# Kernel tuning notes

Measured on AMD Instinct MI355X. Metric: run time of the kernel, lower is better.

Reference implementation:

```python
import jax, jax.numpy as jnp
import numpy as np

N_NODES = 50000
N_EDGES = 1600000
NEG_SLOPE = 0.2


def _gat_layer(x, src, dst, W, a_src, a_dst, b, n_nodes):
    # PyG GATConv (heads=1, concat=True): h = xW; e_ij = LeakyReLU(a_src.h_j + a_dst.h_i)
    # alpha = softmax over incoming edges of each target i; out_i = sum_j alpha_ij h_j + b
    h = x @ W                                   # [N, out]
    alpha_src = h @ a_src                        # [N]
    alpha_dst = h @ a_dst                        # [N]
    e = alpha_src[src] + alpha_dst[dst]          # [E]
    e = jnp.where(e > 0, e, NEG_SLOPE * e)       # leaky_relu(0.2)
    m = jax.ops.segment_max(e, dst, num_segments=n_nodes)   # per-target max
    ex = jnp.exp(e - m[dst])
    denom = jax.ops.segment_sum(ex, dst, num_segments=n_nodes)
    alpha = ex / (denom[dst] + 1e-16)            # [E]
    out = jax.ops.segment_sum(alpha[:, None] * h[src], dst, num_segments=n_nodes)
    return out + b


def setup_inputs() -> dict:
    key = jax.random.key(0)
    ks = jax.random.split(key, 16)
    hid, out_dim, in_dim = 128, 5, 13
    x = jax.random.normal(ks[0], (N_NODES, in_dim), dtype=jnp.float32)
    edge_index = jax.random.randint(ks[1], (2, N_EDGES), 0, N_NODES, dtype=jnp.int64)
    s = 0.1
    return {
        "x": x,
        "edge_index": edge_index,
        "W1": jax.random.normal(ks[2], (in_dim, hid), dtype=jnp.float32) * s,
        "a_src1": jax.random.normal(ks[3], (hid,), dtype=jnp.float32) * s,
        "a_dst1": jax.random.normal(ks[4], (hid,), dtype=jnp.float32) * s,
        "b1": jnp.zeros((hid,), dtype=jnp.float32),
        "W2": jax.random.normal(ks[5], (hid, hid), dtype=jnp.float32) * s,
        "a_src2": jax.random.normal(ks[6], (hid,), dtype=jnp.float32) * s,
        "a_dst2": jax.random.normal(ks[7], (hid,), dtype=jnp.float32) * s,
        "b2": jnp.zeros((hid,), dtype=jnp.float32),
        "W3": jax.random.normal(ks[8], (hid, out_dim), dtype=jnp.float32) * s,
        "a_src3": jax.random.normal(ks[9], (out_dim,), dtype=jnp.float32) * s,
        "a_dst3": jax.random.normal(ks[10], (out_dim,), dtype=jnp.float32) * s,
        "b3": jnp.zeros((out_dim,), dtype=jnp.float32),
    }


def reference(x, edge_index, W1, a_src1, a_dst1, b1, W2, a_src2, a_dst2, b2,
              W3, a_src3, a_dst3, b3):
    n = x.shape[0]
    # GATConv add_self_loops=True: append (i, i) edges
    loops = jnp.arange(n, dtype=edge_index.dtype)
    src = jnp.concatenate([edge_index[0], loops])
    dst = jnp.concatenate([edge_index[1], loops])
    h = _gat_layer(x, src, dst, W1, a_src1, a_dst1, b1, n)
    h = jax.nn.relu(h)  # dropout identity in eval mode
    h = _gat_layer(h, src, dst, W2, a_src2, a_dst2, b2, n)
    h = jax.nn.relu(h)
    h = _gat_layer(h, src, dst, W3, a_src3, a_dst3, b3, n)
    return jax.nn.log_softmax(h, axis=1)
```

## Files before the change

### kernel.cpp

```cpp
#include <hip/hip_runtime.h>
#include <hip/hip_bf16.h>


#define LEAKY(e) ((e) > 0.f ? (e) : 0.2f * (e))
#define CAPB 6144
__device__ inline float clamp30(float e) { return fminf(fmaxf(e, -30.f), 30.f); }
__device__ inline float expc(float e) { return __expf(clamp30(LEAKY(e))); }

__device__ inline float ldany(const void* p, int bf, int i) {
    return bf ? __bfloat162float(((const __hip_bfloat16*)p)[i])
              : ((const float*)p)[i];
}
__device__ inline int ldidx(const void* p, int i64, long long i) {
    return i64 ? (int)(((const unsigned int*)p)[2 * i])
               : ((const int*)p)[i];
}

__device__ inline float bflo(unsigned int w) { return __uint_as_float(w << 16); }
__device__ inline float bfhi(unsigned int w) { return __uint_as_float(w & 0xffff0000u); }
__device__ inline unsigned short bfbits(float a) {
    __hip_bfloat16 x = __float2bfloat16(a);
    unsigned short u; __builtin_memcpy(&u, &x, 2); return u;
}
__device__ inline unsigned int packbf(float a, float b) {
    return (unsigned int)bfbits(a) | ((unsigned int)bfbits(b) << 16);
}

typedef __attribute__((ext_vector_type(8))) short short8;
typedef __attribute__((ext_vector_type(4))) float f32x4;

__global__ void detect_kernel(const void* W1, const void* ei, int* flags) {
    if (threadIdx.x == 0 && blockIdx.x == 0) {
        const unsigned int* w = (const unsigned int*)W1;
        int c = 0;
        for (int i = 0; i < 64; i++) {
            unsigned int e = (w[i] >> 7) & 0xFFu;
            if (e >= 0x70u && e <= 0x7Fu) c++;
        }
        flags[0] = (c >= 32) ? 1 : 0;
        const unsigned int* q = (const unsigned int*)ei;
        int z = 0;
        for (int i = 0; i < 64; i++)
            if (q[2 * i + 1] == 0u) z++;
        flags[1] = (z >= 32) ? 1 : 0;
    }
}


__global__ __launch_bounds__(256) void zero_ints(int* p, int n) {
    int i = blockIdx.x * 256 + threadIdx.x;
    if (i < n) p[i] = 0;
}

__global__ __launch_bounds__(256) void scatter1(
    const void* __restrict__ ei, const int* __restrict__ flags,
    int* __restrict__ gcur, unsigned int* __restrict__ pairbuf, int E, int NBUK)
{
    __shared__ unsigned int ebuf[6400];
    __shared__ int hist[512];
    __shared__ int wbase[512];
    const int i64 = flags[1];
    const int tid = threadIdx.x, blk = blockIdx.x;
    const int chunk = (E + 255) / 256;
    const int e0 = blk * chunk, e1 = min(e0 + chunk, E);
    for (int sub = e0; sub < e1; sub += 6400) {
        const int cnt = min(6400, e1 - sub);
        for (int i = tid; i < NBUK; i += 256) hist[i] = 0;
        __syncthreads();
        for (int i = tid; i < cnt; i += 256) {
            int s = ldidx(ei, i64, sub + i);
            int d = ldidx(ei, i64, (long long)E + sub + i);
            ebuf[i] = ((unsigned int)d << 16) | (unsigned int)s;
            atomicAdd(&hist[d >> 7], 1);
        }
        __syncthreads();
        for (int b = tid; b < NBUK; b += 256) {
            int h = hist[b];
            wbase[b] = (h > 0) ? (b * CAPB + atomicAdd(&gcur[b], h)) : 0;
            hist[b] = 0;
        }
        __syncthreads();
        for (int i = tid; i < cnt; i += 256) {
            unsigned int w = ebuf[i];
            int b = (int)(w >> 23);
            int p = atomicAdd(&hist[b], 1);
            pairbuf[wbase[b] + p] = w;
        }
        __syncthreads();
    }
}

__global__ __launch_bounds__(512) void sortB2_scan(
    const int* __restrict__ gcur, int* __restrict__ bucketBase, int NBUK)
{
    __shared__ int wt[8];
    __shared__ int wbase[8];
    __shared__ int total_s;
    const int tid = threadIdx.x, lane = tid & 63, wid = tid >> 6;
    int v = (tid < NBUK) ? gcur[tid] : 0;
    int x = v;
#pragma unroll
    for (int o = 1; o < 64; o <<= 1) {
        int y = __shfl_up(x, o);
        if (lane >= o) x += y;
    }
    if (lane == 63) wt[wid] = x;
    __syncthreads();
    if (tid == 0) {
        int s = 0;
#pragma unroll
        for (int i = 0; i < 8; i++) { wbase[i] = s; s += wt[i]; }
        total_s = s;
    }
    __syncthreads();
    if (tid < NBUK) bucketBase[tid] = x - v + wbase[wid];
    if (tid == 0) bucketBase[NBUK] = total_s;
}

__global__ __launch_bounds__(256) void sortD_bin(
    const unsigned int* __restrict__ pairbuf, const int* __restrict__ bucketBase,
    int* __restrict__ rowptr, unsigned short* __restrict__ ssrc,
    int N, int NBUK)
{
    __shared__ int cnt[128];
    __shared__ int cur2[128];
    __shared__ int wt1;
    const int b = blockIdx.x;
    const int tid = threadIdx.x, lane = tid & 63;
    const int e0 = bucketBase[b], e1 = bucketBase[b + 1];
    const int nloc = e1 - e0;
    const unsigned int* pb = pairbuf + (size_t)b * CAPB;
    if (tid < 128) cnt[tid] = 0;
    __syncthreads();
    for (int i = tid; i < nloc; i += 256)
        atomicAdd(&cnt[(pb[i] >> 16) & 127], 1);
    __syncthreads();
    if (tid < 128) {
        int v = cnt[tid];
        int x = v;
#pragma unroll
        for (int o = 1; o < 64; o <<= 1) {
            int y = __shfl_up(x, o);
            if (lane >= o) x += y;
        }
        if (tid == 63) wt1 = x;
        __syncthreads();
        if (tid >= 64) x += wt1;
        int pfx = x - v;
        cur2[tid] = pfx;
        int node = b * 128 + tid;
        if (node < N) rowptr[node] = e0 + pfx;
    } else {
        __syncthreads();
    }
    if (b == NBUK - 1 && tid == 0) rowptr[N] = e1;
    __syncthreads();
    for (int i = tid; i < nloc; i += 256) {
        unsigned int w = pb[i];
        int p = atomicAdd(&cur2[(w >> 16) & 127], 1);
        ssrc[e0 + p] = (unsigned short)(w & 0xFFFFu);
    }
}


__global__ __launch_bounds__(256) void node_prep13(
    const void* __restrict__ xin, const void* __restrict__ Wg,
    const void* __restrict__ asg, const void* __restrict__ adg,
    const int* __restrict__ flags,
    unsigned int* __restrict__ h2, float* __restrict__ asrc,
    float* __restrict__ adst, int N)
{
    const int bf = flags[0];
    __shared__ float Wlds[13 * 128];
    for (int i = threadIdx.x; i < 13 * 128; i += 256)
        Wlds[i] = ldany(Wg, bf, i);
    __syncthreads();
    const int lane = threadIdx.x & 63;
    int wave = (blockIdx.x * 256 + threadIdx.x) >> 6;
    int nw = (gridDim.x * 256) >> 6;
    float a0 = ldany(asg, bf, 2 * lane), a1 = ldany(asg, bf, 2 * lane + 1);
    float d0 = ldany(adg, bf, 2 * lane), d1 = ldany(adg, bf, 2 * lane + 1);
    for (int n = wave; n < N; n += nw) {
        float x0 = (lane < 13) ? ldany(xin, bf, n * 13 + lane) : 0.f;
        float s0 = 0.f, s1 = 0.f;
#pragma unroll
        for (int k = 0; k < 13; k++) {
            float xv = __shfl(x0, k);
            s0 += xv * Wlds[k * 128 + 2 * lane];
            s1 += xv * Wlds[k * 128 + 2 * lane + 1];
        }
        float pa = s0 * a0 + s1 * a1;
        float pd = s0 * d0 + s1 * d1;
#pragma unroll
        for (int o = 32; o > 0; o >>= 1) {
            pa += __shfl_xor(pa, o);
            pd += __shfl_xor(pd, o);
        }
        if (lane == 0) { asrc[n] = pa; adst[n] = pd; }
        h2[(size_t)n * 64 + lane] = packbf(s0, s1);
    }
}

__global__ __launch_bounds__(256) void gemm_mfma(
    const float* __restrict__ X, const void* __restrict__ Wg,
    const void* __restrict__ asg, const void* __restrict__ adg,
    const int* __restrict__ flags, unsigned int* __restrict__ h2,
    float* __restrict__ asrc, float* __restrict__ adst, int N)
{
    const int bf = flags[0];
    __shared__ unsigned short A_s[64 * 136];
    __shared__ unsigned short B_s[128 * 136];
    const int tid = threadIdx.x;
    const int nb0 = blockIdx.x * 64;

#pragma unroll
    for (int it = 0; it < 16; it++) {
        int f = it * 256 + tid;
        int k = f >> 5, ng = (f & 31) * 4;
        if (!bf) {
            float4 v = *(const float4*)((const float*)Wg + k * 128 + ng);
            B_s[(ng + 0) * 136 + k] = bfbits(v.x);
            B_s[(ng + 1) * 136 + k] = bfbits(v.y);
            B_s[(ng + 2) * 136 + k] = bfbits(v.z);
            B_s[(ng + 3) * 136 + k] = bfbits(v.w);
        } else {
            const unsigned short* W16 = (const unsigned short*)Wg;
            B_s[(ng + 0) * 136 + k] = W16[k * 128 + ng + 0];
            B_s[(ng + 1) * 136 + k] = W16[k * 128 + ng + 1];
            B_s[(ng + 2) * 136 + k] = W16[k * 128 + ng + 2];
            B_s[(ng + 3) * 136 + k] = W16[k * 128 + ng + 3];
        }
    }
#pragma unroll
    for (int it = 0; it < 8; it++) {
        int f = it * 256 + tid;
        int n = f >> 5, g = f & 31;
        int node = min(nb0 + n, N - 1);
        float4 v = *(const float4*)&X[(size_t)node * 128 + g * 4];
        unsigned int* dst = (unsigned int*)&A_s[n * 136 + g * 4];
        dst[0] = packbf(v.x, v.y);
        dst[1] = packbf(v.z, v.w);
    }
    __syncthreads();

    const int wv = tid >> 6;
    const int lane = tid & 63;
    const int m = lane & 15, quad = lane >> 4;

    f32x4 acc[8];
#pragma unroll
    for (int c = 0; c < 8; c++) acc[c] = (f32x4){0.f, 0.f, 0.f, 0.f};

#pragma unroll
    for (int q = 0; q < 4; q++) {
        short8 a = *(const short8*)&A_s[(wv * 16 + m) * 136 + q * 32 + quad * 8];
#pragma unroll
        for (int c = 0; c < 8; c++) {
            short8 b = *(const short8*)&B_s[(c * 16 + m) * 136 + q * 32 + quad * 8];
            acc[c] = __builtin_amdgcn_mfma_f32_16x16x32_bf16(a, b, acc[c], 0, 0, 0);
        }
    }

    float asv[8], adv[8];
#pragma unroll
    for (int c = 0; c < 8; c++) {
        asv[c] = ldany(asg, bf, c * 16 + m);
        adv[c] = ldany(adg, bf, c * 16 + m);
    }
    unsigned short* h2u = (unsigned short*)h2;
#pragma unroll
    for (int reg = 0; reg < 4; reg++) {
        int node = nb0 + wv * 16 + quad * 4 + reg;
        float pa = 0.f, pd = 0.f;
#pragma unroll
        for (int c = 0; c < 8; c++) {
            float v = acc[c][reg];
            pa += v * asv[c];
            pd += v * adv[c];
            if (node < N) h2u[(size_t)node * 128 + c * 16 + m] = bfbits(v);
        }
#pragma unroll
        for (int o = 1; o < 16; o <<= 1) {
            pa += __shfl_xor(pa, o);
            pd += __shfl_xor(pd, o);
        }
        if (node < N && m == 0) { asrc[node] = pa; adst[node] = pd; }
    }
}

__global__ __launch_bounds__(256) void proj7(
    const float* __restrict__ X, const void* __restrict__ W3,
    const void* __restrict__ as3, const void* __restrict__ ad3,
    const int* __restrict__ flags, float* __restrict__ h3p,
    float* __restrict__ asrc, float* __restrict__ adst, int N)
{
    const int bf = flags[0];
    __shared__ float Wp[128 * 8];
    __shared__ float xs[256 * 33];
    const int tid = threadIdx.x;
    for (int i = tid; i < 128 * 8; i += 256) {
        int k = i >> 3, j = i & 7;
        float v = 0.f;
        if (j < 5) v = ldany(W3, bf, k * 5 + j);
        else if (j == 5) v = ldany(as3, bf, k);
        else if (j == 6) v = ldany(ad3, bf, k);
        Wp[i] = v;
    }
    const int nb0 = blockIdx.x * 256;
    float acc[7] = {0.f, 0.f, 0.f, 0.f, 0.f, 0.f, 0.f};
    for (int kc = 0; kc < 128; kc += 32) {
        __syncthreads();
#pragma unroll
        for (int it = 0; it < 32; it++) {
            int f = it * 256 + tid;
            int row = f >> 5, k = f & 31;
            int node = nb0 + row;
            xs[row * 33 + k] = (node < N) ? X[(size_t)node * 128 + kc + k] : 0.f;
        }
        __syncthreads();
#pragma unroll
        for (int k = 0; k < 32; k++) {
            float xv = xs[tid * 33 + k];
            float4 w0 = *(float4*)&Wp[(kc + k) * 8];
            float4 w1 = *(float4*)&Wp[(kc + k) * 8 + 4];
            acc[0] += xv * w0.x; acc[1] += xv * w0.y; acc[2] += xv * w0.z;
            acc[3] += xv * w0.w; acc[4] += xv * w1.x; acc[5] += xv * w1.y;
            acc[6] += xv * w1.z;
        }
    }
    int node = nb0 + tid;
    if (node < N) {
        float4 o0 = {acc[0], acc[1], acc[2], acc[3]};
        float4 o1 = {acc[4], 0.f, 0.f, 0.f};
        *(float4*)&h3p[(size_t)node * 8] = o0;
        *(float4*)&h3p[(size_t)node * 8 + 4] = o1;
        asrc[node] = acc[5];
        adst[node] = acc[6];
    }
}


__device__ inline int rdl(int v, int j) { return __builtin_amdgcn_readlane(v, j); }
__device__ inline float rdlf(float v, int j) {
    return __uint_as_float((unsigned int)__builtin_amdgcn_readlane((int)__float_as_uint(v), j));
}

__global__ __launch_bounds__(256) void agg_fused128(
    const int* __restrict__ rowptr, const unsigned short* __restrict__ ssrc,
    const unsigned int* __restrict__ h2, const float* __restrict__ asrc,
    const float* __restrict__ adst, const void* __restrict__ bias,
    const int* __restrict__ flags, float* __restrict__ feat, int N)
{
    const int bf = flags[0];
    const int lane = threadIdx.x & 63;
    int wave = (blockIdx.x * 256 + threadIdx.x) >> 6;
    int nw = (gridDim.x * 256) >> 6;
    const float bx = ldany(bias, bf, 2 * lane);
    const float by = ldany(bias, bf, 2 * lane + 1);
    const unsigned ul = (unsigned)lane;

    for (int n = wave; n < N; n += nw) {
        float ad = adst[n];
        float wself = expc(asrc[n] + ad);
        unsigned int hw = h2[((unsigned)n << 6) | ul];
        float accx = wself * bflo(hw), accy = wself * bfhi(hw);
        float wpart = (lane == 0) ? wself : 0.f;
        const int start = rowptr[n], end = rowptr[n + 1];
        for (int base = start; base < end; base += 64) {
            int sl = 0;
            float wl = 0.f;
            if (base + lane < end) {
                sl = (int)ssrc[base + lane];
                wl = expc(asrc[sl] + ad);
            }
            wpart += wl;
            const int cnt = min(64, end - base);
            int j = 0;
            for (; j + 16 <= cnt; j += 16) {
                unsigned int u[16];
                float w[16];
#pragma unroll
                for (int t = 0; t < 16; t++) {
                    unsigned s = (unsigned)rdl(sl, j + t);
                    u[t] = h2[(s << 6) | ul];
                }
#pragma unroll
                for (int t = 0; t < 16; t++) w[t] = rdlf(wl, j + t);
#pragma unroll
                for (int t = 0; t < 16; t++) {
                    accx += w[t] * bflo(u[t]);
                    accy += w[t] * bfhi(u[t]);
                }
            }
            for (; j + 8 <= cnt; j += 8) {
                unsigned int u[8];
                float w[8];
#pragma unroll
                for (int t = 0; t < 8; t++) {
                    unsigned s = (unsigned)rdl(sl, j + t);
                    u[t] = h2[(s << 6) | ul];
                }
#pragma unroll
                for (int t = 0; t < 8; t++) w[t] = rdlf(wl, j + t);
#pragma unroll
                for (int t = 0; t < 8; t++) {
                    accx += w[t] * bflo(u[t]);
                    accy += w[t] * bfhi(u[t]);
                }
            }
            for (; j < cnt; j++) {
                unsigned s = (unsigned)rdl(sl, j);
                float w = rdlf(wl, j);
                unsigned int ww = h2[(s << 6) | ul];
                accx += w * bflo(ww);
                accy += w * bfhi(ww);
            }
        }
        float wsum = wpart;
#pragma unroll
        for (int o = 32; o > 0; o >>= 1) wsum += __shfl_xor(wsum, o);
        float inv = 1.f / (wsum + 1e-16f);
        float2 ov = {fmaxf(accx * inv + bx, 0.f), fmaxf(accy * inv + by, 0.f)};
        *(float2*)&feat[(size_t)n * 128 + 2 * lane] = ov;
    }
}

__global__ __launch_bounds__(256) void agg_fused5(
    const int* __restrict__ rowptr, const unsigned short* __restrict__ ssrc,
    const float* __restrict__ h3p, const float* __restrict__ asrc,
    const float* __restrict__ adst, const void* __restrict__ b3,
    const int* __restrict__ flags, float* __restrict__ out, int N)
{
    const int bf = flags[0];
    const int lane = threadIdx.x & 63;
    int wave = (blockIdx.x * 256 + threadIdx.x) >> 6;
    int nw = (gridDim.x * 256) >> 6;

    for (int n = wave; n < N; n += nw) {
        float ad = adst[n];
        float a0 = 0.f, a1 = 0.f, a2 = 0.f, a3 = 0.f, a4 = 0.f, wsum = 0.f;
        if (lane == 0) {
            float w = expc(asrc[n] + ad);
            wsum = w;
            float4 v = *(const float4*)&h3p[(unsigned)n * 8u];
            float v4 = h3p[(unsigned)n * 8u + 4u];
            a0 = w * v.x; a1 = w * v.y; a2 = w * v.z; a3 = w * v.w; a4 = w * v4;
        }
        const int start = rowptr[n], end = rowptr[n + 1];
        for (int i = start + lane; i < end; i += 64) {
            unsigned s = (unsigned)ssrc[i];
            float w = expc(asrc[s] + ad);
            float4 v = *(const float4*)&h3p[s * 8u];
            float v4 = h3p[s * 8u + 4u];
            wsum += w;
            a0 += w * v.x; a1 += w * v.y; a2 += w * v.z; a3 += w * v.w; a4 += w * v4;
        }
#pragma unroll
        for (int o = 32; o > 0; o >>= 1) {
            a0 += __shfl_xor(a0, o); a1 += __shfl_xor(a1, o); a2 += __shfl_xor(a2, o);
            a3 += __shfl_xor(a3, o); a4 += __shfl_xor(a4, o); wsum += __shfl_xor(wsum, o);
        }
        if (lane == 0) {
            float inv = 1.f / (wsum + 1e-16f);
            float v0 = a0 * inv + ldany(b3, bf, 0);
            float v1 = a1 * inv + ldany(b3, bf, 1);
            float v2 = a2 * inv + ldany(b3, bf, 2);
            float v3 = a3 * inv + ldany(b3, bf, 3);
            float v4 = a4 * inv + ldany(b3, bf, 4);
            float m = fmaxf(fmaxf(fmaxf(v0, v1), fmaxf(v2, v3)), v4);
            float s = __expf(v0 - m) + __expf(v1 - m) + __expf(v2 - m)
                    + __expf(v3 - m) + __expf(v4 - m);
            float lse = m + __logf(s);
            out[n * 5 + 0] = v0 - lse; out[n * 5 + 1] = v1 - lse;
            out[n * 5 + 2] = v2 - lse; out[n * 5 + 3] = v3 - lse;
            out[n * 5 + 4] = v4 - lse;
        }
    }
}

extern "C" void kernel_launch(void* const* d_in, const int* in_sizes, int n_in,
                              void* d_out, int out_size, void* d_ws, size_t ws_size,
                              hipStream_t stream)
{
    const void* x  = d_in[0];
    const void* ei = d_in[1];
    const void* W1 = d_in[2];
    const void* as1= d_in[3];
    const void* ad1= d_in[4];
    const void* b1 = d_in[5];
    const void* W2 = d_in[6];
    const void* as2= d_in[7];
    const void* ad2= d_in[8];
    const void* b2 = d_in[9];
    const void* W3 = d_in[10];
    const void* as3= d_in[11];
    const void* ad3= d_in[12];
    const void* b3 = d_in[13];

    const int N = in_sizes[0] / 13;
    const int E = in_sizes[1] / 2;
    const int NBUK = (N + 127) / 128;

    float* ws    = (float*)d_ws;
    float* feat  = ws;
    unsigned int* h2 = (unsigned int*)(feat + (size_t)N * 128);
    float* asrc  = (float*)(h2 + (size_t)N * 64);
    float* adst  = asrc + N;
    float* h3p   = adst + N;
    int*   rowptr= (int*)(h3p + (size_t)N * 8);
    int*   bucketBase = rowptr + N + 1;
    int*   gcur  = bucketBase + NBUK + 1;
    unsigned int* pairbuf = (unsigned int*)(gcur + NBUK);
    unsigned short* ssrc16 = (unsigned short*)(pairbuf + (size_t)NBUK * CAPB);
    int*   flags = (int*)(ssrc16 + E);

    const int wb = (N + 3) / 4;
    const int gb = (N + 63) / 64;
    const int pb = (N + 255) / 256;

    detect_kernel<<<1, 64, 0, stream>>>(W1, ei, flags);

    zero_ints<<<(NBUK + 255) / 256, 256, 0, stream>>>(gcur, NBUK);
    scatter1<<<256, 256, 0, stream>>>(ei, flags, gcur, pairbuf, E, NBUK);
    sortB2_scan<<<1, 512, 0, stream>>>(gcur, bucketBase, NBUK);
    sortD_bin<<<NBUK, 256, 0, stream>>>(pairbuf, bucketBase, rowptr, ssrc16, N, NBUK);

    node_prep13<<<1024, 256, 0, stream>>>(x, W1, as1, ad1, flags, h2, asrc, adst, N);
    agg_fused128<<<wb, 256, 0, stream>>>(rowptr, ssrc16, h2, asrc, adst, b1, flags, feat, N);

    gemm_mfma<<<gb, 256, 0, stream>>>(feat, W2, as2, ad2, flags, h2, asrc, adst, N);
    agg_fused128<<<wb, 256, 0, stream>>>(rowptr, ssrc16, h2, asrc, adst, b2, flags, feat, N);

    proj7<<<pb, 256, 0, stream>>>(feat, W3, as3, ad3, flags, h3p, asrc, adst, N);
    agg_fused5<<<wb, 256, 0, stream>>>(rowptr, ssrc16, h3p, asrc, adst, b3, flags,
                                       (float*)d_out, N);
}
```

Measured before the change: 340.3 us.

## Replace capped bucket scatter with hist-prefix-scatter sort, pack bf16 weight with src index

The edge bucketing changes from a fixed-capacity per-bucket buffer filled through global atomics to a three-pass counting sort: per-block histograms, a per-bucket prefix over blocks, then a scatter into exact offsets. This removes the CAPB overflow risk and the padded pairbuf, at the cost of reading the edge list twice and launching extra kernels. In the aggregation kernel, the attention weight is rounded to bf16 and packed with the 16-bit source index into one register, so each neighbour needs a single readlane instead of two. This lowers weight precision, and the middle unroll step drops from 8 to 4.

```diff
diff --git a/kernel.cpp b/kernel.cpp
--- a/kernel.cpp
+++ b/kernel.cpp
@@ -3,7 +3,6 @@
 
 
 #define LEAKY(e) ((e) > 0.f ? (e) : 0.2f * (e))
-#define CAPB 6144
 __device__ inline float clamp30(float e) { return fminf(fmaxf(e, -30.f), 30.f); }
 __device__ inline float expc(float e) { return __expf(clamp30(LEAKY(e))); }
 
@@ -47,57 +46,60 @@
 }
 
 
-__global__ __launch_bounds__(256) void zero_ints(int* p, int n) {
-    int i = blockIdx.x * 256 + threadIdx.x;
-    if (i < n) p[i] = 0;
-}
-
-__global__ __launch_bounds__(256) void scatter1(
+__global__ __launch_bounds__(256) void sortA_hist(
     const void* __restrict__ ei, const int* __restrict__ flags,
-    int* __restrict__ gcur, unsigned int* __restrict__ pairbuf, int E, int NBUK)
-{
-    __shared__ unsigned int ebuf[6400];
+    int* __restrict__ blockHist, int E, int NBUK)
+{
     __shared__ int hist[512];
-    __shared__ int wbase[512];
     const int i64 = flags[1];
     const int tid = threadIdx.x, blk = blockIdx.x;
+    for (int i = tid; i < NBUK; i += 256) hist[i] = 0;
+    __syncthreads();
     const int chunk = (E + 255) / 256;
     const int e0 = blk * chunk, e1 = min(e0 + chunk, E);
-    for (int sub = e0; sub < e1; sub += 6400) {
-        const int cnt = min(6400, e1 - sub);
-        for (int i = tid; i < NBUK; i += 256) hist[i] = 0;
-        __syncthreads();
-        for (int i = tid; i < cnt; i += 256) {
-            int s = ldidx(ei, i64, sub + i);
-            int d = ldidx(ei, i64, (long long)E + sub + i);
-            ebuf[i] = ((unsigned int)d << 16) | (unsigned int)s;
-            atomicAdd(&hist[d >> 7], 1);
-        }
-        __syncthreads();
-        for (int b = tid; b < NBUK; b += 256) {
-            int h = hist[b];
-            wbase[b] = (h > 0) ? (b * CAPB + atomicAdd(&gcur[b], h)) : 0;
-            hist[b] = 0;
-        }
-        __syncthreads();
-        for (int i = tid; i < cnt; i += 256) {
-            unsigned int w = ebuf[i];
-            int b = (int)(w >> 23);
-            int p = atomicAdd(&hist[b], 1);
-            pairbuf[wbase[b] + p] = w;
-        }
-        __syncthreads();
-    }
+    for (int t = e0 + tid; t < e1; t += 256) {
+        int d = ldidx(ei, i64, (long long)E + t);
+        atomicAdd(&hist[d >> 7], 1);
+    }
+    __syncthreads();
+    for (int i = tid; i < NBUK; i += 256)
+        blockHist[blk * NBUK + i] = hist[i];
+}
+
+__global__ __launch_bounds__(256) void sortB_prefix(
+    int* __restrict__ blockHist, int* __restrict__ bucketBase, int NBUK)
+{
+    __shared__ int wt[4];
+    __shared__ int wbase[4];
+    const int b = blockIdx.x;
+    const int tid = threadIdx.x, lane = tid & 63, wid = tid >> 6;
+    int v = blockHist[tid * NBUK + b];
+    int x = v;
+#pragma unroll
+    for (int o = 1; o < 64; o <<= 1) {
+        int y = __shfl_up(x, o);
+        if (lane >= o) x += y;
+    }
+    if (lane == 63) wt[wid] = x;
+    __syncthreads();
+    if (tid == 0) {
+        int s = 0;
+#pragma unroll
+        for (int i = 0; i < 4; i++) { wbase[i] = s; s += wt[i]; }
+        bucketBase[b] = s;
+    }
+    __syncthreads();
+    blockHist[tid * NBUK + b] = x - v + wbase[wid];
 }
 
 __global__ __launch_bounds__(512) void sortB2_scan(
-    const int* __restrict__ gcur, int* __restrict__ bucketBase, int NBUK)
+    int* __restrict__ bucketBase, int NBUK)
 {
     __shared__ int wt[8];
     __shared__ int wbase[8];
     __shared__ int total_s;
     const int tid = threadIdx.x, lane = tid & 63, wid = tid >> 6;
-    int v = (tid < NBUK) ? gcur[tid] : 0;
+    int v = (tid < NBUK) ? bucketBase[tid] : 0;
     int x = v;
 #pragma unroll
     for (int o = 1; o < 64; o <<= 1) {
@@ -117,10 +119,30 @@
     if (tid == 0) bucketBase[NBUK] = total_s;
 }
 
+__global__ __launch_bounds__(256) void sortC_scatter(
+    const void* __restrict__ ei, const int* __restrict__ flags,
+    const int* __restrict__ blockHist, const int* __restrict__ bucketBase,
+    unsigned int* __restrict__ pairbuf, int E, int NBUK)
+{
+    __shared__ int cur[512];
+    const int i64 = flags[1];
+    const int tid = threadIdx.x, blk = blockIdx.x;
+    for (int i = tid; i < NBUK; i += 256)
+        cur[i] = blockHist[blk * NBUK + i] + bucketBase[i];
+    __syncthreads();
+    const int chunk = (E + 255) / 256;
+    const int e0 = blk * chunk, e1 = min(e0 + chunk, E);
+    for (int t = e0 + tid; t < e1; t += 256) {
+        int s = ldidx(ei, i64, t);
+        int d = ldidx(ei, i64, (long long)E + t);
+        int pos = atomicAdd(&cur[d >> 7], 1);
+        pairbuf[pos] = ((unsigned int)(d & 127) << 16) | (unsigned int)s;
+    }
+}
+
 __global__ __launch_bounds__(256) void sortD_bin(
     const unsigned int* __restrict__ pairbuf, const int* __restrict__ bucketBase,
-    int* __restrict__ rowptr, unsigned short* __restrict__ ssrc,
-    int N, int NBUK)
+    int* __restrict__ rowptr, unsigned short* __restrict__ ssrc, int N, int NBUK)
 {
     __shared__ int cnt[128];
     __shared__ int cur2[128];
@@ -128,12 +150,10 @@
     const int b = blockIdx.x;
     const int tid = threadIdx.x, lane = tid & 63;
     const int e0 = bucketBase[b], e1 = bucketBase[b + 1];
-    const int nloc = e1 - e0;
-    const unsigned int* pb = pairbuf + (size_t)b * CAPB;
     if (tid < 128) cnt[tid] = 0;
     __syncthreads();
-    for (int i = tid; i < nloc; i += 256)
-        atomicAdd(&cnt[(pb[i] >> 16) & 127], 1);
+    for (int i = e0 + tid; i < e1; i += 256)
+        atomicAdd(&cnt[pairbuf[i] >> 16], 1);
     __syncthreads();
     if (tid < 128) {
         int v = cnt[tid];
@@ -155,9 +175,9 @@
     }
     if (b == NBUK - 1 && tid == 0) rowptr[N] = e1;
     __syncthreads();
-    for (int i = tid; i < nloc; i += 256) {
-        unsigned int w = pb[i];
-        int p = atomicAdd(&cur2[(w >> 16) & 127], 1);
+    for (int i = e0 + tid; i < e1; i += 256) {
+        unsigned int w = pairbuf[i];
+        int p = atomicAdd(&cur2[w >> 16], 1);
         ssrc[e0 + p] = (unsigned short)(w & 0xFFFFu);
     }
 }
@@ -340,9 +360,8 @@
 }
 
 
-__device__ inline int rdl(int v, int j) { return __builtin_amdgcn_readlane(v, j); }
-__device__ inline float rdlf(float v, int j) {
-    return __uint_as_float((unsigned int)__builtin_amdgcn_readlane((int)__float_as_uint(v), j));
+__device__ inline unsigned rdlu(unsigned v, int j) {
+    return (unsigned)__builtin_amdgcn_readlane((int)v, j);
 }
 
 __global__ __launch_bounds__(256) void agg_fused128(
@@ -367,51 +386,55 @@
         float wpart = (lane == 0) ? wself : 0.f;
         const int start = rowptr[n], end = rowptr[n + 1];
         for (int base = start; base < end; base += 64) {
-            int sl = 0;
-            float wl = 0.f;
+            unsigned pkl = 0;
             if (base + lane < end) {
-                sl = (int)ssrc[base + lane];
-                wl = expc(asrc[sl] + ad);
+                unsigned s = (unsigned)ssrc[base + lane];
+                float wl = expc(asrc[s] + ad);
+                unsigned wb = ((unsigned)bfbits(wl)) << 16;
+                wpart += __uint_as_float(wb);
+                pkl = wb | s;
             }
-            wpart += wl;
             const int cnt = min(64, end - base);
             int j = 0;
             for (; j + 16 <= cnt; j += 16) {
-                unsigned int u[16];
-                float w[16];
+                unsigned pk[16];
+                unsigned u[16];
+#pragma unroll
+                for (int t = 0; t < 16; t++) pk[t] = rdlu(pkl, j + t);
 #pragma unroll
                 for (int t = 0; t < 16; t++) {
-                    unsigned s = (unsigned)rdl(sl, j + t);
-                    u[t] = h2[(s << 6) | ul];
+                    const unsigned int* row = h2 + ((pk[t] & 0xFFFFu) << 6);
+                    u[t] = row[ul];
                 }
 #pragma unroll
-                for (int t = 0; t < 16; t++) w[t] = rdlf(wl, j + t);
-#pragma unroll
                 for (int t = 0; t < 16; t++) {
-                    accx += w[t] * bflo(u[t]);
-                    accy += w[t] * bfhi(u[t]);
+                    float w = __uint_as_float(pk[t] & 0xFFFF0000u);
+                    accx += w * bflo(u[t]);
+                    accy += w * bfhi(u[t]);
                 }
             }
-            for (; j + 8 <= cnt; j += 8) {
-                unsigned int u[8];
-                float w[8];
-#pragma unroll
-                for (int t = 0; t < 8; t++) {
-                    unsigned s = (unsigned)rdl(sl, j + t);
-                    u[t] = h2[(s << 6) | ul];
+            for (; j + 4 <= cnt; j += 4) {
+                unsigned pk[4];
+                unsigned u[4];
+#pragma unroll
+                for (int t = 0; t < 4; t++) pk[t] = rdlu(pkl, j + t);
+#pragma unroll
+                for (int t = 0; t < 4; t++) {
+                    const unsigned int* row = h2 + ((pk[t] & 0xFFFFu) << 6);
+                    u[t] = row[ul];
                 }
 #pragma unroll
-                for (int t = 0; t < 8; t++) w[t] = rdlf(wl, j + t);
-#pragma unroll
-                for (int t = 0; t < 8; t++) {
-                    accx += w[t] * bflo(u[t]);
-                    accy += w[t] * bfhi(u[t]);
+                for (int t = 0; t < 4; t++) {
+                    float w = __uint_as_float(pk[t] & 0xFFFF0000u);
+                    accx += w * bflo(u[t]);
+                    accy += w * bfhi(u[t]);
                 }
             }
             for (; j < cnt; j++) {
-                unsigned s = (unsigned)rdl(sl, j);
-                float w = rdlf(wl, j);
-                unsigned int ww = h2[(s << 6) | ul];
+                unsigned pk = rdlu(pkl, j);
+                const unsigned int* row = h2 + ((pk & 0xFFFFu) << 6);
+                unsigned ww = row[ul];
+                float w = __uint_as_float(pk & 0xFFFF0000u);
                 accx += w * bflo(ww);
                 accy += w * bfhi(ww);
             }
@@ -509,9 +532,9 @@
     float* h3p   = adst + N;
     int*   rowptr= (int*)(h3p + (size_t)N * 8);
     int*   bucketBase = rowptr + N + 1;
-    int*   gcur  = bucketBase + NBUK + 1;
-    unsigned int* pairbuf = (unsigned int*)(gcur + NBUK);
-    unsigned short* ssrc16 = (unsigned short*)(pairbuf + (size_t)NBUK * CAPB);
+    int*   blockHist  = bucketBase + NBUK + 1;
+    unsigned int* pairbuf = (unsigned int*)(blockHist + 256 * NBUK);
+    unsigned short* ssrc16 = (unsigned short*)(pairbuf + E);
     int*   flags = (int*)(ssrc16 + E);
 
     const int wb = (N + 3) / 4;
@@ -520,9 +543,11 @@
 
     detect_kernel<<<1, 64, 0, stream>>>(W1, ei, flags);
 
-    zero_ints<<<(NBUK + 255) / 256, 256, 0, stream>>>(gcur, NBUK);
-    scatter1<<<256, 256, 0, stream>>>(ei, flags, gcur, pairbuf, E, NBUK);
-    sortB2_scan<<<1, 512, 0, stream>>>(gcur, bucketBase, NBUK);
+    sortA_hist<<<256, 256, 0, stream>>>(ei, flags, blockHist, E, NBUK);
+    sortB_prefix<<<NBUK, 256, 0, stream>>>(blockHist, bucketBase, NBUK);
+    sortB2_scan<<<1, 512, 0, stream>>>(bucketBase, NBUK);
+    sortC_scatter<<<256, 256, 0, stream>>>(ei, flags, blockHist, bucketBase,
+                                           pairbuf, E, NBUK);
     sortD_bin<<<NBUK, 256, 0, stream>>>(pairbuf, bucketBase, rowptr, ssrc16, N, NBUK);
 
     node_prep13<<<1024, 256, 0, stream>>>(x, W1, as1, ad1, flags, h2, asrc, adst, N);
```

Measured after the change: 338.6 us. Within noise of the previous version (-0.5%).
